# Kernel optimization log

Hardware: AMD Instinct MI355X
Metric: run time of the kernel (lower is better)

Reference implementation:

```python
import jax, jax.numpy as jnp
import numpy as np

T, B, C, H, W = 9, 8, 256, 56, 56


def setup_inputs() -> dict:
    key = jax.random.key(0)
    k1, k2, k3, k4 = jax.random.split(key, 4)
    feature_maps_sequence = jax.random.normal(k1, (T, B, C, H, W), dtype=jnp.float32)
    # Conv2d(2C, 1, kernel_size=1): weight [1, 2C, 1, 1], bias [1]
    w = jax.random.normal(k2, (1, 2 * C, 1, 1), dtype=jnp.float32) * 0.02
    b = jax.random.normal(k3, (1,), dtype=jnp.float32) * 0.02
    gamma = jax.random.normal(k4, (1,), dtype=jnp.float32)
    return {"feature_maps_sequence": feature_maps_sequence, "w": w, "b": b, "gamma": gamma}


def reference(feature_maps_sequence, w, b, gamma):
    seq = feature_maps_sequence  # [T, B, C, H, W]
    t = seq.shape[0]
    center = seq[t // 2]  # [B, C, H, W]
    c = seq.shape[2]
    # 1x1 conv over concat([center, frame]) == dot with split weight halves + bias
    w_center = w[0, :c, 0, 0]  # [C]
    w_other = w[0, c:, 0, 0]   # [C]
    score_center = jnp.einsum('bchw,c->bhw', center, w_center)          # [B, H, W]
    score_other = jnp.einsum('tbchw,c->tbhw', seq, w_other)             # [T, B, H, W]
    scores = score_center[None] + score_other + b[0]                    # [T, B, H, W]
    attn = jax.nn.softmax(scores, axis=0)                               # softmax over T
    attended = jnp.einsum('tbhw,tbchw->bchw', attn, seq)                # [B, C, H, W]
    return center + gamma * attended
```

## Files before the change

kernel.cpp:

```cpp
#include <hip/hip_runtime.h>
#include <math.h>

#define TT 9
#define BN 8
#define CC 256
#define HW 3136
#define P 8
#define NCHUNK (HW / P)
#define CENTER_T 4

__global__ __launch_bounds__(256) void fused_stage_kernel(
    const float* __restrict__ seq, const float* __restrict__ w,
    const float* __restrict__ gamma, float* __restrict__ out) {
  int blk = blockIdx.x;
  int b = blk & 7;
  int chunk = blk >> 3;
  int px0 = chunk * P;
  int tid = threadIdx.x;

  __shared__ __align__(16) float tile[TT * CC * P];
  __shared__ float wsh[CC];
  __shared__ float red[TT * P * 4];
  __shared__ __align__(16) float sc[TT * P];

  wsh[tid] = w[CC + tid];

  {
    const int c_lo = tid >> 1;
    const int g = (tid & 1) * 4;
    const int fsw = ((c_lo >> 2) & 7) << 2;
    const int wbase = (8 * c_lo + g) ^ fsw;
    const float* sgb = seq + (size_t)b * CC * HW + (size_t)c_lo * HW + g + px0;
#pragma unroll
    for (int k = 0; k < 18; ++k) {
      const int koff = (k >> 1) * (BN * CC * HW) + (k & 1) * (128 * HW);
      float4 v = *(const float4*)(sgb + koff);
      *(float4*)(&tile[wbase + (k >> 1) * 2048 + (k & 1) * 1024]) = v;
    }
  }
  __syncthreads();

  for (int v = tid; v < 288; v += 256) {
    const int pair = v >> 2;
    const int cp = v & 3;
    const int t = pair >> 3;
    const int px = pair & 7;
    const int sbase = t * 2048 + cp * 8 + px;
    float a = 0.f;
#pragma unroll
    for (int i = 0; i < 64; ++i)
      a = fmaf(tile[(sbase ^ ((i & 7) << 2)) + 32 * i], wsh[cp + 4 * i], a);
    red[v] = a;
  }
  __syncthreads();

  if (tid < P) {
    float vv[TT];
    float m = -1e30f;
#pragma unroll
    for (int t = 0; t < TT; ++t) {
      const int pr = (t * P + tid) * 4;
      const float s = red[pr] + red[pr + 1] + red[pr + 2] + red[pr + 3];
      vv[t] = s;
      m = fmaxf(m, s);
    }
    float s = 0.f;
#pragma unroll
    for (int t = 0; t < TT; ++t) { vv[t] = __expf(vv[t] - m); s += vv[t]; }
    const float inv = 1.f / s;
#pragma unroll
    for (int t = 0; t < TT; ++t) sc[t * P + tid] = vv[t] * inv;
  }
  __syncthreads();

  {
    const int c = tid;
    const int f2 = ((c >> 2) & 7) << 2;
    const int abase0 = (8 * c) ^ f2;
    const int abase4 = (8 * c + 4) ^ f2;
    float4 o0 = {0.f, 0.f, 0.f, 0.f}, o1 = {0.f, 0.f, 0.f, 0.f};
    float4 c0v = {0.f, 0.f, 0.f, 0.f}, c1v = {0.f, 0.f, 0.f, 0.f};
#pragma unroll
    for (int t = 0; t < TT; ++t) {
      const float4 s0 = *(const float4*)(&sc[t * P]);
      const float4 s1 = *(const float4*)(&sc[t * P + 4]);
      const float4 v0 = *(const float4*)(&tile[abase0 + t * 2048]);
      const float4 v1 = *(const float4*)(&tile[abase4 + t * 2048]);
      o0.x = fmaf(s0.x, v0.x, o0.x);
      o0.y = fmaf(s0.y, v0.y, o0.y);
      o0.z = fmaf(s0.z, v0.z, o0.z);
      o0.w = fmaf(s0.w, v0.w, o0.w);
      o1.x = fmaf(s1.x, v1.x, o1.x);
      o1.y = fmaf(s1.y, v1.y, o1.y);
      o1.z = fmaf(s1.z, v1.z, o1.z);
      o1.w = fmaf(s1.w, v1.w, o1.w);
      if (t == CENTER_T) { c0v = v0; c1v = v1; }
    }
    const float gm = gamma[0];
    float4 r0, r1;
    r0.x = fmaf(gm, o0.x, c0v.x);
    r0.y = fmaf(gm, o0.y, c0v.y);
    r0.z = fmaf(gm, o0.z, c0v.z);
    r0.w = fmaf(gm, o0.w, c0v.w);
    r1.x = fmaf(gm, o1.x, c1v.x);
    r1.y = fmaf(gm, o1.y, c1v.y);
    r1.z = fmaf(gm, o1.z, c1v.z);
    r1.w = fmaf(gm, o1.w, c1v.w);
    float* ob = out + ((size_t)b * CC + c) * HW + px0;
    *(float4*)(ob) = r0;
    *(float4*)(ob + 4) = r1;
  }
}

extern "C" void kernel_launch(void* const* d_in, const int* in_sizes, int n_in,
                              void* d_out, int out_size, void* d_ws, size_t ws_size,
                              hipStream_t stream) {
  const float* seq = (const float*)d_in[0];
  const float* w = (const float*)d_in[1];
  const float* gamma = (const float*)d_in[3];
  float* out = (float*)d_out;

  fused_stage_kernel<<<BN * NCHUNK, 256, 0, stream>>>(seq, w, gamma, out);
}
```

Before: 344.3 us.

## Halve pixel chunk to 4 and restructure tile load, swizzle and reduction

Each block now handles 4 pixels instead of 8. That halves shared memory per block (about 37KB instead of 74KB), and launch bounds now request 4 blocks per CU to raise occupancy. The global load now issues all 9 timestep float4 loads up front, and the shared tile gets a new XOR swizzle with a matching dot-product indexing scheme. The risk is that each global access becomes 16-byte segments strided across channels, which lowers coalescing, and the grid doubles to twice as many blocks.

```diff
diff --git a/kernel.cpp b/kernel.cpp
--- a/kernel.cpp
+++ b/kernel.cpp
@@ -5,62 +5,61 @@
 #define BN 8
 #define CC 256
 #define HW 3136
-#define P 8
+#define P 4
 #define NCHUNK (HW / P)
 #define CENTER_T 4
 
-__global__ __launch_bounds__(256) void fused_stage_kernel(
+__global__ __launch_bounds__(256, 4) void fused_stage_kernel(
     const float* __restrict__ seq, const float* __restrict__ w,
     const float* __restrict__ gamma, float* __restrict__ out) {
-  int blk = blockIdx.x;
-  int b = blk & 7;
-  int chunk = blk >> 3;
-  int px0 = chunk * P;
-  int tid = threadIdx.x;
+  const int blk = blockIdx.x;
+  const int b = blk & 7;
+  const int chunk = blk >> 3;
+  const int px0 = chunk * P;
+  const int tid = threadIdx.x;
 
   __shared__ __align__(16) float tile[TT * CC * P];
   __shared__ float wsh[CC];
-  __shared__ float red[TT * P * 4];
+  __shared__ __align__(16) float red[36 * 4];
   __shared__ __align__(16) float sc[TT * P];
 
   wsh[tid] = w[CC + tid];
 
   {
-    const int c_lo = tid >> 1;
-    const int g = (tid & 1) * 4;
-    const int fsw = ((c_lo >> 2) & 7) << 2;
-    const int wbase = (8 * c_lo + g) ^ fsw;
-    const float* sgb = seq + (size_t)b * CC * HW + (size_t)c_lo * HW + g + px0;
+    const float* sgb = seq + ((size_t)b * CC + tid) * HW + px0;
+    float4 pre[TT];
 #pragma unroll
-    for (int k = 0; k < 18; ++k) {
-      const int koff = (k >> 1) * (BN * CC * HW) + (k & 1) * (128 * HW);
-      float4 v = *(const float4*)(sgb + koff);
-      *(float4*)(&tile[wbase + (k >> 1) * 2048 + (k & 1) * 1024]) = v;
-    }
+    for (int t = 0; t < TT; ++t)
+      pre[t] = *(const float4*)(sgb + (size_t)t * (BN * CC * HW));
+#pragma unroll
+    for (int t = 0; t < TT; ++t)
+      *(float4*)(&tile[(t * 1024 + 4 * tid) ^ ((t & 1) << 4)]) = pre[t];
   }
   __syncthreads();
 
-  for (int v = tid; v < 288; v += 256) {
-    const int pair = v >> 2;
-    const int cp = v & 3;
-    const int t = pair >> 3;
-    const int px = pair & 7;
-    const int sbase = t * 2048 + cp * 8 + px;
+  if (tid < 144) {
+    const int cp = tid & 3;
+    const int pair = tid >> 2;
+    const int t = pair >> 2;
+    const int px = pair & 3;
+    const int e = t & 1;
+    const int sbase = t * 1024 + 4 * cp + px;
     float a = 0.f;
 #pragma unroll
-    for (int i = 0; i < 64; ++i)
-      a = fmaf(tile[(sbase ^ ((i & 7) << 2)) + 32 * i], wsh[cp + 4 * i], a);
-    red[v] = a;
+    for (int j = 0; j < 64; ++j)
+      a = fmaf(tile[sbase + 16 * j], wsh[cp + 4 * (j ^ e)], a);
+    red[tid] = a;
   }
   __syncthreads();
 
   if (tid < P) {
+    const int px = tid;
     float vv[TT];
     float m = -1e30f;
 #pragma unroll
     for (int t = 0; t < TT; ++t) {
-      const int pr = (t * P + tid) * 4;
-      const float s = red[pr] + red[pr + 1] + red[pr + 2] + red[pr + 3];
+      const float4 r = *(const float4*)(&red[(t * 4 + px) * 4]);
+      const float s = (r.x + r.y) + (r.z + r.w);
       vv[t] = s;
       m = fmaxf(m, s);
     }
@@ -69,46 +68,32 @@
     for (int t = 0; t < TT; ++t) { vv[t] = __expf(vv[t] - m); s += vv[t]; }
     const float inv = 1.f / s;
 #pragma unroll
-    for (int t = 0; t < TT; ++t) sc[t * P + tid] = vv[t] * inv;
+    for (int t = 0; t < TT; ++t) sc[t * P + px] = vv[t] * inv;
   }
   __syncthreads();
 
   {
     const int c = tid;
-    const int f2 = ((c >> 2) & 7) << 2;
-    const int abase0 = (8 * c) ^ f2;
-    const int abase4 = (8 * c + 4) ^ f2;
-    float4 o0 = {0.f, 0.f, 0.f, 0.f}, o1 = {0.f, 0.f, 0.f, 0.f};
-    float4 c0v = {0.f, 0.f, 0.f, 0.f}, c1v = {0.f, 0.f, 0.f, 0.f};
+    float4 o = {0.f, 0.f, 0.f, 0.f};
+    float4 cv = {0.f, 0.f, 0.f, 0.f};
 #pragma unroll
     for (int t = 0; t < TT; ++t) {
-      const float4 s0 = *(const float4*)(&sc[t * P]);
-      const float4 s1 = *(const float4*)(&sc[t * P + 4]);
-      const float4 v0 = *(const float4*)(&tile[abase0 + t * 2048]);
-      const float4 v1 = *(const float4*)(&tile[abase4 + t * 2048]);
-      o0.x = fmaf(s0.x, v0.x, o0.x);
-      o0.y = fmaf(s0.y, v0.y, o0.y);
-      o0.z = fmaf(s0.z, v0.z, o0.z);
-      o0.w = fmaf(s0.w, v0.w, o0.w);
-      o1.x = fmaf(s1.x, v1.x, o1.x);
-      o1.y = fmaf(s1.y, v1.y, o1.y);
-      o1.z = fmaf(s1.z, v1.z, o1.z);
-      o1.w = fmaf(s1.w, v1.w, o1.w);
-      if (t == CENTER_T) { c0v = v0; c1v = v1; }
+      const float4 s = *(const float4*)(&sc[t * P]);
+      const float4 v = *(const float4*)(&tile[(t * 1024 + 4 * c) ^ ((t & 1) << 4)]);
+      o.x = fmaf(s.x, v.x, o.x);
+      o.y = fmaf(s.y, v.y, o.y);
+      o.z = fmaf(s.z, v.z, o.z);
+      o.w = fmaf(s.w, v.w, o.w);
+      if (t == CENTER_T) cv = v;
     }
     const float gm = gamma[0];
-    float4 r0, r1;
-    r0.x = fmaf(gm, o0.x, c0v.x);
-    r0.y = fmaf(gm, o0.y, c0v.y);
-    r0.z = fmaf(gm, o0.z, c0v.z);
-    r0.w = fmaf(gm, o0.w, c0v.w);
-    r1.x = fmaf(gm, o1.x, c1v.x);
-    r1.y = fmaf(gm, o1.y, c1v.y);
-    r1.z = fmaf(gm, o1.z, c1v.z);
-    r1.w = fmaf(gm, o1.w, c1v.w);
+    float4 r;
+    r.x = fmaf(gm, o.x, cv.x);
+    r.y = fmaf(gm, o.y, cv.y);
+    r.z = fmaf(gm, o.z, cv.z);
+    r.w = fmaf(gm, o.w, cv.w);
     float* ob = out + ((size_t)b * CC + c) * HW + px0;
-    *(float4*)(ob) = r0;
-    *(float4*)(ob + 4) = r1;
+    *(float4*)(ob) = r;
   }
 }
 
```

Result: slower. 363.0 us (+5.4%).
